# Optimization experiments

Hardware: AMD Instinct MI355X
Metric: run time of the kernel (lower is better)

Reference implementation:

```python
import jax, jax.numpy as jnp
import numpy as np

N_HEAD = 12

def setup_inputs() -> dict:
    key = jax.random.key(0)
    ks = jax.random.split(key, 5)
    B, T, C = 4, 2048, 768
    scale = 0.02
    return {
        "x": jax.random.normal(ks[0], (B, T, C), dtype=jnp.float32),
        "W_attn": jax.random.normal(ks[1], (C, 3 * C), dtype=jnp.float32) * scale,
        "b_attn": jax.random.normal(ks[2], (3 * C,), dtype=jnp.float32) * scale,
        "W_proj": jax.random.normal(ks[3], (C, C), dtype=jnp.float32) * scale,
        "b_proj": jax.random.normal(ks[4], (C,), dtype=jnp.float32) * scale,
    }

def reference(x, W_attn, b_attn, W_proj, b_proj):
    B, T, C = x.shape
    H = N_HEAD
    D = C // H  # head dim
    qkv = x @ W_attn + b_attn  # [B,T,3C]
    q, k, v = jnp.split(qkv, 3, axis=-1)
    # [B,H,T,D]
    q = q.reshape(B, T, H, D).transpose(0, 2, 1, 3)
    k = k.reshape(B, T, H, D).transpose(0, 2, 1, 3)
    v = v.reshape(B, T, H, D).transpose(0, 2, 1, 3)
    scores = jnp.einsum('bhqd,bhkd->bhqk', q, k) / jnp.sqrt(jnp.float32(D))
    causal = jnp.tril(jnp.ones((T, T), dtype=bool))
    scores = jnp.where(causal[None, None, :, :], scores, jnp.float32(-jnp.inf))
    attn = jax.nn.softmax(scores, axis=-1)
    out = jnp.einsum('bhqk,bhkd->bhqd', attn, v)  # [B,H,T,D]
    out = out.transpose(0, 2, 1, 3).reshape(B, T, C)
    return out @ W_proj + b_proj
```

## Files before the change

### kernel.cpp

```cpp
#include <hip/hip_runtime.h>

typedef float f32x4 __attribute__((ext_vector_type(4)));
typedef __bf16 bf16x8 __attribute__((ext_vector_type(8)));
typedef unsigned short u16x8 __attribute__((ext_vector_type(8)));
typedef unsigned short u16x4 __attribute__((ext_vector_type(4)));

#define MFMA16(a, b, c) __builtin_amdgcn_mfma_f32_16x16x32_bf16((a), (b), (c), 0, 0, 0)

__device__ __forceinline__ unsigned short f2bf(float f) {
    __bf16 h = (__bf16)f;
    union { __bf16 h; unsigned short u; } c; c.h = h;
    return c.u;
}

__device__ __forceinline__ void gload_lds16(const unsigned short* g, unsigned short* l) {
    __builtin_amdgcn_global_load_lds(
        (const __attribute__((address_space(1))) unsigned int*)g,
        (__attribute__((address_space(3))) unsigned int*)l, 16, 0, 0);
}

__global__ void k_convert_bf16(const float* __restrict__ in,
                               unsigned short* __restrict__ out, int n) {
    int i = (blockIdx.x * 256 + threadIdx.x) * 4;
    if (i + 3 < n) {
        float4 v = *reinterpret_cast<const float4*>(in + i);
        ushort4 o;
        o.x = f2bf(v.x); o.y = f2bf(v.y); o.z = f2bf(v.z); o.w = f2bf(v.w);
        *reinterpret_cast<ushort4*>(out + i) = o;
    }
}

__global__ void k_transpose_bf16(const float* __restrict__ in,
                                 unsigned short* __restrict__ out, int R, int C) {
    __shared__ unsigned short tile[32][33];
    int bx = blockIdx.x * 32;
    int by = blockIdx.y * 32;
    int tx = threadIdx.x;
    int ty = threadIdx.y;
    #pragma unroll
    for (int i = ty; i < 32; i += 8)
        tile[i][tx] = f2bf(in[(size_t)(by + i) * C + bx + tx]);
    __syncthreads();
    #pragma unroll
    for (int i = ty; i < 32; i += 8)
        out[(size_t)(bx + i) * R + by + tx] = tile[tx][i];
}

__global__ __launch_bounds__(512) void k_gemm_qkv(
    const unsigned short* __restrict__ A,
    const unsigned short* __restrict__ Bt,
    const float* __restrict__ bias,
    unsigned short* __restrict__ Qo,
    unsigned short* __restrict__ Ko,
    unsigned short* __restrict__ Vto,
    int K)
{
    __shared__ unsigned short SM[2 * 16384 + 2 * 8192];
    const int nwg = gridDim.x * gridDim.y;
    const int bid0 = blockIdx.y * gridDim.x + blockIdx.x;
    const int logical = (bid0 & 7) * (nwg >> 3) + (bid0 >> 3);
    const int bm = logical / gridDim.x;
    const int bn = logical % gridDim.x;
    const int tid = threadIdx.x;
    const int w = tid >> 6, l = tid & 63;
    const int wm = w >> 1, wn = w & 1;
    const int ln = l & 15, kb = l >> 4;

    f32x4 acc[4][4];
    #pragma unroll
    for (int i = 0; i < 4; ++i)
        #pragma unroll
        for (int j = 0; j < 4; ++j)
            #pragma unroll
            for (int r = 0; r < 4; ++r) acc[i][j][r] = 0.f;

    const unsigned short* Ab = A + (size_t)(bm * 256) * K;
    const unsigned short* Bb = Bt + (size_t)(bn * 128) * K;

    const int srow = tid >> 3;
    const int sslot = tid & 7;
    const int csw = (sslot ^ (srow & 7)) * 8;

    #define QSTAGE(t_, buf_)                                                        \
        {                                                                           \
            const int k0_ = (t_) * 64;                                              \
            _Pragma("unroll")                                                       \
            for (int j = 0; j < 4; ++j) {                                           \
                const int r = j * 64 + srow;                                        \
                gload_lds16(&Ab[(size_t)r * K + k0_ + csw],                         \
                            &SM[(buf_) * 16384 + r * 64 + sslot * 8]);              \
            }                                                                       \
            _Pragma("unroll")                                                       \
            for (int j = 0; j < 2; ++j) {                                           \
                const int r = j * 64 + srow;                                        \
                gload_lds16(&Bb[(size_t)r * K + k0_ + csw],                         \
                            &SM[32768 + (buf_) * 8192 + r * 64 + sslot * 8]);       \
            }                                                                       \
        }

    QSTAGE(0, 0);
    __syncthreads();

    for (int t = 0; t < 12; ++t) {
        const int buf = t & 1;
        if (t + 1 < 12) QSTAGE(t + 1, buf ^ 1);
        #pragma unroll
        for (int kh = 0; kh < 2; ++kh) {
            bf16x8 af[4], bfr[4];
            #pragma unroll
            for (int mt = 0; mt < 4; ++mt) {
                const int row = wm * 64 + mt * 16 + ln;
                const int slot = ((kh << 2) | kb) ^ (row & 7);
                af[mt] = *reinterpret_cast<const bf16x8*>(
                    &SM[buf * 16384 + row * 64 + slot * 8]);
            }
            #pragma unroll
            for (int nt = 0; nt < 4; ++nt) {
                const int row = wn * 64 + nt * 16 + ln;
                const int slot = ((kh << 2) | kb) ^ (row & 7);
                bfr[nt] = *reinterpret_cast<const bf16x8*>(
                    &SM[32768 + buf * 8192 + row * 64 + slot * 8]);
            }
            #pragma unroll
            for (int mt = 0; mt < 4; ++mt)
                #pragma unroll
                for (int nt = 0; nt < 4; ++nt)
                    acc[mt][nt] = MFMA16(af[mt], bfr[nt], acc[mt][nt]);
        }
        __syncthreads();
    }

    const float SC = 0.1803368801111204f;

    if (bn >= 12) {
        unsigned short* Ts = SM;
        const int cl_w = wn * 64;
        #pragma unroll
        for (int hh2 = 0; hh2 < 2; ++hh2) {
            if ((wm >> 1) == hh2) {
                #pragma unroll
                for (int mt = 0; mt < 4; ++mt) {
                    #pragma unroll
                    for (int nt = 0; nt < 4; ++nt) {
                        const int cl = cl_w + nt * 16 + ln;
                        const float bv = bias[bn * 128 + cl];
                        #pragma unroll
                        for (int r = 0; r < 4; ++r) {
                            const int rl = (wm & 1) * 64 + mt * 16 + kb * 4 + r;
                            const int pos = cl * 128 + ((((rl >> 3) ^ (cl & 7)) << 3) | (rl & 7));
                            Ts[pos] = f2bf(acc[mt][nt][r] + bv);
                        }
                    }
                }
            }
            __syncthreads();
            {
                const int cl = tid >> 2;
                const int col = bn * 128 + cl;
                const int cc = col - 1536;
                const int hh = cc >> 6, dd = cc & 63;
                #pragma unroll
                for (int j8 = 0; j8 < 4; ++j8) {
                    const int rb = (tid & 3) * 4 + j8;
                    u16x8 val = *reinterpret_cast<const u16x8*>(&Ts[cl * 128 + ((rb ^ (cl & 7)) << 3)]);
                    const int tg = bm * 256 + hh2 * 128 + rb * 8;
                    const int bb = tg >> 11;
                    const int tloc = tg & 2047;
                    const int grp = tloc & ~31;
                    const int jj = (tloc >> 3) & 3;
                    const int tlo = grp + 8 * ((2 * jj) & 3) + 4 * (jj >> 1);
                    const int thi = grp + 8 * ((2 * jj + 1) & 3) + 4 * (jj >> 1);
                    unsigned short* basep = &Vto[((size_t)((bb * 12 + hh) * 64 + dd)) * 2048];
                    *reinterpret_cast<u16x4*>(basep + tlo) =
                        __builtin_shufflevector(val, val, 0, 1, 2, 3);
                    *reinterpret_cast<u16x4*>(basep + thi) =
                        __builtin_shufflevector(val, val, 4, 5, 6, 7);
                }
            }
            __syncthreads();
        }
        return;
    }

    #pragma unroll
    for (int mt = 0; mt < 4; ++mt) {
        #pragma unroll
        for (int nt = 0; nt < 4; ++nt) {
            const int col = bn * 128 + wn * 64 + nt * 16 + ln;
            #pragma unroll
            for (int r = 0; r < 4; ++r) {
                const int row = bm * 256 + wm * 64 + mt * 16 + kb * 4 + r;
                float v = acc[mt][nt][r] + bias[col];
                int cc = col >= 768 ? col - 768 : col;
                int h = cc >> 6, d = cc & 63;
                int b = row >> 11, t = row & 2047;
                if (col < 768)
                    Qo[((size_t)((b * 12 + h) * 2048 + t)) * 64 + d] = f2bf(v * SC);
                else
                    Ko[((size_t)((b * 12 + h) * 2048 + t)) * 64 + d] = f2bf(v);
            }
        }
    }
    #undef QSTAGE
}

__global__ __launch_bounds__(256) void k_gemm_proj(
    const unsigned short* __restrict__ A,
    const unsigned short* __restrict__ Bt,
    const float* __restrict__ bias,
    float* __restrict__ Co,
    int K)
{
    constexpr int BM = 128;
    __shared__ unsigned short SM[(BM + 128) * 64];
    unsigned short* As = SM;
    unsigned short* Bs = SM + BM * 64;
    const int nwg = gridDim.x * gridDim.y;
    const int bid0 = blockIdx.y * gridDim.x + blockIdx.x;
    const int logical = (bid0 & 7) * (nwg >> 3) + (bid0 >> 3);
    const int bm = logical / gridDim.x;
    const int bn = logical % gridDim.x;
    const int tid = threadIdx.x;
    const int w = tid >> 6, l = tid & 63;
    const int wm = w >> 1, wn = w & 1;
    const int ln = l & 15, kb = l >> 4;

    f32x4 acc[4][4];
    #pragma unroll
    for (int i = 0; i < 4; ++i)
        #pragma unroll
        for (int j = 0; j < 4; ++j)
            #pragma unroll
            for (int r = 0; r < 4; ++r) acc[i][j][r] = 0.f;

    const unsigned short* Ab = A + (size_t)(bm * BM) * K;
    const unsigned short* Bb = Bt + (size_t)(bn * 128) * K;

    const int srow = tid >> 3;
    const int sslot = tid & 7;
    const int csw = (sslot ^ (srow & 7)) * 8;

    for (int k0 = 0; k0 < K; k0 += 64) {
        #pragma unroll
        for (int j = 0; j < 4; ++j) {
            const int r = j * 32 + srow;
            gload_lds16(&Ab[(size_t)r * K + k0 + csw], &As[r * 64 + sslot * 8]);
        }
        #pragma unroll
        for (int j = 0; j < 4; ++j) {
            const int r = j * 32 + srow;
            gload_lds16(&Bb[(size_t)r * K + k0 + csw], &Bs[r * 64 + sslot * 8]);
        }
        __syncthreads();
        #pragma unroll
        for (int kh = 0; kh < 2; ++kh) {
            bf16x8 af[4], bfr[4];
            #pragma unroll
            for (int mt = 0; mt < 4; ++mt) {
                const int row = wm * 64 + mt * 16 + ln;
                const int slot = ((kh << 2) | kb) ^ (row & 7);
                af[mt] = *reinterpret_cast<const bf16x8*>(&As[row * 64 + slot * 8]);
            }
            #pragma unroll
            for (int nt = 0; nt < 4; ++nt) {
                const int row = wn * 64 + nt * 16 + ln;
                const int slot = ((kh << 2) | kb) ^ (row & 7);
                bfr[nt] = *reinterpret_cast<const bf16x8*>(&Bs[row * 64 + slot * 8]);
            }
            #pragma unroll
            for (int mt = 0; mt < 4; ++mt)
                #pragma unroll
                for (int nt = 0; nt < 4; ++nt)
                    acc[mt][nt] = MFMA16(af[mt], bfr[nt], acc[mt][nt]);
        }
        __syncthreads();
    }

    #pragma unroll
    for (int mt = 0; mt < 4; ++mt) {
        #pragma unroll
        for (int nt = 0; nt < 4; ++nt) {
            const int col = bn * 128 + wn * 64 + nt * 16 + ln;
            #pragma unroll
            for (int r = 0; r < 4; ++r) {
                const int row = bm * BM + wm * 64 + mt * 16 + kb * 4 + r;
                Co[(size_t)row * 768 + col] = acc[mt][nt][r] + bias[col];
            }
        }
    }
}

__global__ __launch_bounds__(256) void k_attn(
    const unsigned short* __restrict__ Q,
    const unsigned short* __restrict__ Kk,
    const unsigned short* __restrict__ Vt,
    unsigned short* __restrict__ Oo)
{
    __shared__ unsigned short SMEM[4 * 4096];
    const int bid0 = blockIdx.x;
    const int xcd = bid0 & 7;
    const int loc = bid0 >> 3;
    const int qb = 15 - (loc / 6);
    const int bh = xcd * 6 + (loc % 6);
    const int tid = threadIdx.x;
    const int w = tid >> 6, l = tid & 63;
    const int ln = l & 15, kb = l >> 4;
    const int kbq = kb * 4;
    const int b = bh / 12, h = bh - b * 12;
    const int q0w = qb * 128 + w * 32;

    const unsigned short* Qb = Q + (size_t)bh * 2048 * 64;
    const unsigned short* Kb = Kk + (size_t)bh * 2048 * 64;
    const unsigned short* Vb = Vt + (size_t)bh * 64 * 2048;

    bf16x8 qf[2][2];
    #pragma unroll
    for (int qn = 0; qn < 2; ++qn) {
        const unsigned short* qr = &Qb[(size_t)(q0w + qn * 16 + ln) * 64 + kb * 8];
        qf[qn][0] = *reinterpret_cast<const bf16x8*>(qr);
        qf[qn][1] = *reinterpret_cast<const bf16x8*>(qr + 32);
    }

    bf16x8 vones;
    #pragma unroll
    for (int e = 0; e < 8; ++e) vones[e] = (__bf16)1.0f;
    const f32x4 fzero = {0.f, 0.f, 0.f, 0.f};

    f32x4 oaccT[2][4];
    f32x4 den[2];
    #pragma unroll
    for (int qn = 0; qn < 2; ++qn) {
        #pragma unroll
        for (int r = 0; r < 4; ++r) den[qn][r] = 0.f;
        #pragma unroll
        for (int dt = 0; dt < 4; ++dt)
            #pragma unroll
            for (int r = 0; r < 4; ++r) oaccT[qn][dt][r] = 0.f;
    }

    const int lb = ln & 7;
    const int aR0 = ln * 64 + (kb ^ lb) * 8;
    const int aR1 = ln * 64 + ((4 | kb) ^ lb) * 8;

    const int srow = tid >> 3;
    const int sslot = tid & 7;
    const int csw = (sslot ^ (srow & 7)) * 8;
    const int lastkt = (q0w + 31) >> 6;

    #define STAGE(kt_, buf_)                                                        \
        {                                                                           \
            const int kb_ = (kt_) * 64;                                             \
            _Pragma("unroll")                                                       \
            for (int j = 0; j < 2; ++j) {                                           \
                const int r = j * 32 + srow;                                        \
                gload_lds16(&Kb[(size_t)(kb_ + r) * 64 + csw],                      \
                            &SMEM[(buf_) * 4096 + r * 64 + sslot * 8]);             \
                gload_lds16(&Vb[(size_t)r * 2048 + kb_ + csw],                      \
                            &SMEM[8192 + (buf_) * 4096 + r * 64 + sslot * 8]);      \
            }                                                                       \
        }

    #define COMPUTE(kt_, BUF)                                                       \
        if ((kt_) <= lastkt) {                                                      \
            bf16x8 kf[4][2];                                                        \
            _Pragma("unroll")                                                       \
            for (int km = 0; km < 4; ++km) {                                        \
                kf[km][0] = *reinterpret_cast<const bf16x8*>(                       \
                    &SMEM[(BUF) * 4096 + km * 1024 + aR0]);                         \
                kf[km][1] = *reinterpret_cast<const bf16x8*>(                       \
                    &SMEM[(BUF) * 4096 + km * 1024 + aR1]);                         \
            }                                                                       \
            f32x4 st[4][2];                                                         \
            _Pragma("unroll")                                                       \
            for (int km = 0; km < 4; ++km)                                          \
                _Pragma("unroll")                                                   \
                for (int qn = 0; qn < 2; ++qn) {                                    \
                    st[km][qn] = MFMA16(kf[km][0], qf[qn][0], fzero);               \
                    st[km][qn] = MFMA16(kf[km][1], qf[qn][1], st[km][qn]);          \
                }                                                                   \
            bf16x8 vf[4][2];                                                        \
            _Pragma("unroll")                                                       \
            for (int dt = 0; dt < 4; ++dt) {                                        \
                vf[dt][0] = *reinterpret_cast<const bf16x8*>(                       \
                    &SMEM[8192 + (BUF) * 4096 + dt * 1024 + aR0]);                  \
                vf[dt][1] = *reinterpret_cast<const bf16x8*>(                       \
                    &SMEM[8192 + (BUF) * 4096 + dt * 1024 + aR1]);                  \
            }                                                                       \
            if ((kt_) == lastkt) {                                                  \
                const int kbase_ = (kt_) * 64;                                      \
                _Pragma("unroll")                                                   \
                for (int qn = 0; qn < 2; ++qn) {                                    \
                    const int qrow = q0w + qn * 16 + ln;                            \
                    _Pragma("unroll")                                               \
                    for (int km = 0; km < 4; ++km)                                  \
                        _Pragma("unroll")                                           \
                        for (int r = 0; r < 4; ++r) {                               \
                            float sv = st[km][qn][r];                               \
                            const int key = kbase_ + km * 16 + kbq + r;             \
                            sv = (key <= qrow) ? sv : -1e30f;                       \
                            st[km][qn][r] = __builtin_amdgcn_exp2f(sv);             \
                        }                                                           \
                }                                                                   \
            } else {                                                                \
                _Pragma("unroll")                                                   \
                for (int qn = 0; qn < 2; ++qn)                                      \
                    _Pragma("unroll")                                               \
                    for (int km = 0; km < 4; ++km)                                  \
                        _Pragma("unroll")                                           \
                        for (int r = 0; r < 4; ++r)                                 \
                            st[km][qn][r] =                                         \
                                __builtin_amdgcn_exp2f(st[km][qn][r]);              \
            }                                                                       \
            bf16x8 pa[2][2];                                                        \
            _Pragma("unroll")                                                       \
            for (int qn = 0; qn < 2; ++qn)                                          \
                _Pragma("unroll")                                                   \
                for (int kh = 0; kh < 2; ++kh) {                                    \
                    bf16x8 t;                                                       \
                    _Pragma("unroll")                                               \
                    for (int r = 0; r < 4; ++r) {                                   \
                        t[r]     = (__bf16)st[2 * kh][qn][r];                       \
                        t[r + 4] = (__bf16)st[2 * kh + 1][qn][r];                   \
                    }                                                               \
                    pa[qn][kh] = t;                                                 \
                }                                                                   \
            _Pragma("unroll")                                                       \
            for (int qn = 0; qn < 2; ++qn) {                                        \
                _Pragma("unroll")                                                   \
                for (int dt = 0; dt < 4; ++dt) {                                    \
                    oaccT[qn][dt] = MFMA16(pa[qn][0], vf[dt][0], oaccT[qn][dt]);    \
                    oaccT[qn][dt] = MFMA16(pa[qn][1], vf[dt][1], oaccT[qn][dt]);    \
                }                                                                   \
                den[qn] = MFMA16(pa[qn][0], vones, den[qn]);                        \
                den[qn] = MFMA16(pa[qn][1], vones, den[qn]);                        \
            }                                                                       \
        }

    STAGE(0, 0);

    for (int s = 0; s <= qb; ++s) {
        const int ktA = 2 * s;
        const int ktB = 2 * s + 1;
        __syncthreads();
        STAGE(ktB, 1);
        COMPUTE(ktA, 0);
        __syncthreads();
        if (s < qb) STAGE(ktA + 2, 0);
        COMPUTE(ktB, 1);
    }

    #pragma unroll
    for (int qn = 0; qn < 2; ++qn) {
        #pragma unroll
        for (int r = 0; r < 4; ++r) {
            const float inv = 1.0f / den[qn][r];
            const int t = q0w + qn * 16 + kbq + r;
            #pragma unroll
            for (int dt = 0; dt < 4; ++dt)
                Oo[((size_t)(b * 2048 + t)) * 768 + h * 64 + dt * 16 + ln] =
                    f2bf(oaccT[qn][dt][r] * inv);
        }
    }
    #undef STAGE
    #undef COMPUTE
}

extern "C" void kernel_launch(void* const* d_in, const int* in_sizes, int n_in,
                              void* d_out, int out_size, void* d_ws, size_t ws_size,
                              hipStream_t stream) {
    const float* x      = (const float*)d_in[0];
    const float* W_attn = (const float*)d_in[1];
    const float* b_attn = (const float*)d_in[2];
    const float* W_proj = (const float*)d_in[3];
    const float* b_proj = (const float*)d_in[4];
    float* out = (float*)d_out;

    char* ws = (char*)d_ws;
    const size_t SZ_X  = (size_t)8192 * 768 * 2;
    const size_t SZ_WA = (size_t)2304 * 768 * 2;
    const size_t SZ_WP = (size_t)768 * 768 * 2;
    const size_t SZ_T  = (size_t)8192 * 768 * 2;

    unsigned short* x_bf = (unsigned short*)(ws);
    unsigned short* wa_t = (unsigned short*)(ws + SZ_X);
    unsigned short* wp_t = (unsigned short*)(ws + SZ_X + SZ_WA);
    unsigned short* Qb   = (unsigned short*)(ws + SZ_X + SZ_WA + SZ_WP);
    unsigned short* Kb   = (unsigned short*)(ws + SZ_X + SZ_WA + SZ_WP + SZ_T);
    unsigned short* Vtb  = (unsigned short*)(ws + SZ_X + SZ_WA + SZ_WP + 2 * SZ_T);
    unsigned short* attn_o = x_bf;

    k_convert_bf16<<<6144, 256, 0, stream>>>(x, x_bf, 8192 * 768);
    dim3 tb(32, 8);
    k_transpose_bf16<<<dim3(2304 / 32, 768 / 32), tb, 0, stream>>>(W_attn, wa_t, 768, 2304);
    k_transpose_bf16<<<dim3(768 / 32, 768 / 32), tb, 0, stream>>>(W_proj, wp_t, 768, 768);
    k_gemm_qkv<<<dim3(18, 32), 512, 0, stream>>>(x_bf, wa_t, b_attn, Qb, Kb, Vtb, 768);
    k_attn<<<768, 256, 0, stream>>>(Qb, Kb, Vtb, attn_o);
    k_gemm_proj<<<dim3(6, 64), 256, 0, stream>>>(attn_o, wp_t, b_proj, out, 768);
}
```

Baseline: 119.2 us.

## Fuse x fp32-to-bf16 conversion into QKV GEMM and merge weight transposes

Drops the separate kernel that converts x to bf16. The QKV GEMM now loads fp32 x straight into registers, converts it, and writes swizzled bf16 into LDS, with the global loads for the next stage issued before the MFMA loop and the LDS write after it. The two weight-transpose launches are merged into one kernel. This removes a full bf16 copy of x in memory and two launches, but each GEMM block now reads twice the A-side bytes (fp32 instead of bf16) and re-reads x across the 18 column blocks. It also uses more registers and VGPR-staged loads instead of direct global-to-LDS transfers.

```diff
diff --git a/kernel.cpp b/kernel.cpp
--- a/kernel.cpp
+++ b/kernel.cpp
@@ -19,41 +19,33 @@
         (__attribute__((address_space(3))) unsigned int*)l, 16, 0, 0);
 }
 
-__global__ void k_convert_bf16(const float* __restrict__ in,
-                               unsigned short* __restrict__ out, int n) {
-    int i = (blockIdx.x * 256 + threadIdx.x) * 4;
-    if (i + 3 < n) {
-        float4 v = *reinterpret_cast<const float4*>(in + i);
-        ushort4 o;
-        o.x = f2bf(v.x); o.y = f2bf(v.y); o.z = f2bf(v.z); o.w = f2bf(v.w);
-        *reinterpret_cast<ushort4*>(out + i) = o;
-    }
-}
-
-__global__ void k_transpose_bf16(const float* __restrict__ in,
-                                 unsigned short* __restrict__ out, int R, int C) {
+__global__ void k_prep(const float* __restrict__ Wa, unsigned short* __restrict__ WaT,
+                       const float* __restrict__ Wp, unsigned short* __restrict__ WpT) {
     __shared__ unsigned short tile[32][33];
-    int bx = blockIdx.x * 32;
-    int by = blockIdx.y * 32;
-    int tx = threadIdx.x;
-    int ty = threadIdx.y;
+    const int seg = (blockIdx.x < 72) ? 0 : 1;
+    const float* in = seg ? Wp : Wa;
+    unsigned short* out = seg ? WpT : WaT;
+    const int C = seg ? 768 : 2304;
+    const int bx = (seg ? (blockIdx.x - 72) : blockIdx.x) * 32;
+    const int by = blockIdx.y * 32;
+    const int tx = threadIdx.x;
+    const int ty = threadIdx.y;
     #pragma unroll
     for (int i = ty; i < 32; i += 8)
         tile[i][tx] = f2bf(in[(size_t)(by + i) * C + bx + tx]);
     __syncthreads();
     #pragma unroll
     for (int i = ty; i < 32; i += 8)
-        out[(size_t)(bx + i) * R + by + tx] = tile[tx][i];
+        out[(size_t)(bx + i) * 768 + by + tx] = tile[tx][i];
 }
 
 __global__ __launch_bounds__(512) void k_gemm_qkv(
-    const unsigned short* __restrict__ A,
+    const float* __restrict__ Ax,
     const unsigned short* __restrict__ Bt,
     const float* __restrict__ bias,
     unsigned short* __restrict__ Qo,
     unsigned short* __restrict__ Ko,
-    unsigned short* __restrict__ Vto,
-    int K)
+    unsigned short* __restrict__ Vto)
 {
     __shared__ unsigned short SM[2 * 16384 + 2 * 8192];
     const int nwg = gridDim.x * gridDim.y;
@@ -74,36 +66,64 @@
             #pragma unroll
             for (int r = 0; r < 4; ++r) acc[i][j][r] = 0.f;
 
-    const unsigned short* Ab = A + (size_t)(bm * 256) * K;
-    const unsigned short* Bb = Bt + (size_t)(bn * 128) * K;
+    const float* Ab = Ax + (size_t)(bm * 256) * 768;
+    const unsigned short* Bb = Bt + (size_t)(bn * 128) * 768;
 
     const int srow = tid >> 3;
     const int sslot = tid & 7;
     const int csw = (sslot ^ (srow & 7)) * 8;
-
-    #define QSTAGE(t_, buf_)                                                        \
+    const int ac = tid & 7;
+    const int ascol = (ac ^ (srow & 7)) * 8;
+
+    float4 av[4][2];
+
+    #define ALOAD(t_)                                                               \
+        {                                                                           \
+            const int k0_ = (t_) * 64 + ac * 8;                                     \
+            _Pragma("unroll")                                                       \
+            for (int j = 0; j < 4; ++j) {                                           \
+                const float* p = &Ab[(size_t)(j * 64 + srow) * 768 + k0_];          \
+                av[j][0] = *reinterpret_cast<const float4*>(p);                     \
+                av[j][1] = *reinterpret_cast<const float4*>(p + 4);                 \
+            }                                                                       \
+        }
+
+    #define AWRITE(buf_)                                                            \
+        {                                                                           \
+            _Pragma("unroll")                                                       \
+            for (int j = 0; j < 4; ++j) {                                           \
+                u16x8 o;                                                            \
+                o[0] = f2bf(av[j][0].x); o[1] = f2bf(av[j][0].y);                   \
+                o[2] = f2bf(av[j][0].z); o[3] = f2bf(av[j][0].w);                   \
+                o[4] = f2bf(av[j][1].x); o[5] = f2bf(av[j][1].y);                   \
+                o[6] = f2bf(av[j][1].z); o[7] = f2bf(av[j][1].w);                   \
+                *reinterpret_cast<u16x8*>(                                          \
+                    &SM[(buf_) * 16384 + (j * 64 + srow) * 64 + ascol]) = o;        \
+            }                                                                       \
+        }
+
+    #define BSTAGE(t_, buf_)                                                        \
         {                                                                           \
             const int k0_ = (t_) * 64;                                              \
             _Pragma("unroll")                                                       \
-            for (int j = 0; j < 4; ++j) {                                           \
-                const int r = j * 64 + srow;                                        \
-                gload_lds16(&Ab[(size_t)r * K + k0_ + csw],                         \
-                            &SM[(buf_) * 16384 + r * 64 + sslot * 8]);              \
-            }                                                                       \
-            _Pragma("unroll")                                                       \
             for (int j = 0; j < 2; ++j) {                                           \
                 const int r = j * 64 + srow;                                        \
-                gload_lds16(&Bb[(size_t)r * K + k0_ + csw],                         \
+                gload_lds16(&Bb[(size_t)r * 768 + k0_ + csw],                       \
                             &SM[32768 + (buf_) * 8192 + r * 64 + sslot * 8]);       \
             }                                                                       \
         }
 
-    QSTAGE(0, 0);
+    BSTAGE(0, 0);
+    ALOAD(0);
+    AWRITE(0);
     __syncthreads();
 
     for (int t = 0; t < 12; ++t) {
         const int buf = t & 1;
-        if (t + 1 < 12) QSTAGE(t + 1, buf ^ 1);
+        if (t + 1 < 12) {
+            BSTAGE(t + 1, buf ^ 1);
+            ALOAD(t + 1);
+        }
         #pragma unroll
         for (int kh = 0; kh < 2; ++kh) {
             bf16x8 af[4], bfr[4];
@@ -127,6 +147,7 @@
                 for (int nt = 0; nt < 4; ++nt)
                     acc[mt][nt] = MFMA16(af[mt], bfr[nt], acc[mt][nt]);
         }
+        if (t + 1 < 12) AWRITE(buf ^ 1);
         __syncthreads();
     }
 
@@ -201,7 +222,9 @@
             }
         }
     }
-    #undef QSTAGE
+    #undef ALOAD
+    #undef AWRITE
+    #undef BSTAGE
 }
 
 __global__ __launch_bounds__(256) void k_gemm_proj(
@@ -476,24 +499,20 @@
     float* out = (float*)d_out;
 
     char* ws = (char*)d_ws;
-    const size_t SZ_X  = (size_t)8192 * 768 * 2;
+    const size_t SZ_AO = (size_t)8192 * 768 * 2;
     const size_t SZ_WA = (size_t)2304 * 768 * 2;
     const size_t SZ_WP = (size_t)768 * 768 * 2;
     const size_t SZ_T  = (size_t)8192 * 768 * 2;
 
-    unsigned short* x_bf = (unsigned short*)(ws);
-    unsigned short* wa_t = (unsigned short*)(ws + SZ_X);
-    unsigned short* wp_t = (unsigned short*)(ws + SZ_X + SZ_WA);
-    unsigned short* Qb   = (unsigned short*)(ws + SZ_X + SZ_WA + SZ_WP);
-    unsigned short* Kb   = (unsigned short*)(ws + SZ_X + SZ_WA + SZ_WP + SZ_T);
-    unsigned short* Vtb  = (unsigned short*)(ws + SZ_X + SZ_WA + SZ_WP + 2 * SZ_T);
-    unsigned short* attn_o = x_bf;
-
-    k_convert_bf16<<<6144, 256, 0, stream>>>(x, x_bf, 8192 * 768);
-    dim3 tb(32, 8);
-    k_transpose_bf16<<<dim3(2304 / 32, 768 / 32), tb, 0, stream>>>(W_attn, wa_t, 768, 2304);
-    k_transpose_bf16<<<dim3(768 / 32, 768 / 32), tb, 0, stream>>>(W_proj, wp_t, 768, 768);
-    k_gemm_qkv<<<dim3(18, 32), 512, 0, stream>>>(x_bf, wa_t, b_attn, Qb, Kb, Vtb, 768);
+    unsigned short* attn_o = (unsigned short*)(ws);
+    unsigned short* wa_t = (unsigned short*)(ws + SZ_AO);
+    unsigned short* wp_t = (unsigned short*)(ws + SZ_AO + SZ_WA);
+    unsigned short* Qb   = (unsigned short*)(ws + SZ_AO + SZ_WA + SZ_WP);
+    unsigned short* Kb   = (unsigned short*)(ws + SZ_AO + SZ_WA + SZ_WP + SZ_T);
+    unsigned short* Vtb  = (unsigned short*)(ws + SZ_AO + SZ_WA + SZ_WP + 2 * SZ_T);
+
+    k_prep<<<dim3(96, 24), dim3(32, 8), 0, stream>>>(W_attn, wa_t, W_proj, wp_t);
+    k_gemm_qkv<<<dim3(18, 32), 512, 0, stream>>>(x, wa_t, b_attn, Qb, Kb, Vtb);
     k_attn<<<768, 256, 0, stream>>>(Qb, Kb, Vtb, attn_o);
     k_gemm_proj<<<dim3(6, 64), 256, 0, stream>>>(attn_o, wp_t, b_proj, out, 768);
 }
```

New measurement: 144.1 us. 20.9% more time.
